# Kernel optimization log

Hardware: AMD Instinct MI355X
Metric: run time of the kernel (lower is better)

Reference implementation:

```python
import jax, jax.numpy as jnp
import numpy as np

N = 100000      # nodes
E = 1600000     # edges (avg degree 16)
F_IN = 128      # input feature dim (lazy in_channels=-1)
HID = 256       # hidden_channels
OUT = 128       # out_channels
NCLS = 2        # final softmax classes


def _l2norm(x):
    # F.normalize(p=2, dim=-1) with eps clamp, as SAGEConv(normalize=True)
    n = jnp.linalg.norm(x, axis=-1, keepdims=True)
    return x / jnp.maximum(n, 1e-12)


def _sage(x, src, tgt, Wl, bl, Wr, n_nodes):
    # PyG SAGEConv: mean-aggregate source features at targets, then
    # out = lin_l(mean_aggr) + lin_r(x); lin_l has bias, lin_r does not.
    s = jax.ops.segment_sum(x[src], tgt, num_segments=n_nodes)          # [N, F]
    cnt = jax.ops.segment_sum(jnp.ones((src.shape[0],), x.dtype), tgt,
                              num_segments=n_nodes)                     # [N]
    mean = s / jnp.maximum(cnt, 1.0)[:, None]
    out = mean @ Wl.T + bl + x @ Wr.T
    return _l2norm(out)


def setup_inputs() -> dict:
    key = jax.random.key(0)
    ks = jax.random.split(key, 12)

    def glorot(k, o, i):
        lim = float(np.sqrt(6.0 / (o + i)))
        return jax.random.uniform(k, (o, i), jnp.float32, -lim, lim)

    return {
        "x": jax.random.normal(ks[0], (N, F_IN), jnp.float32),
        "edge_index": jax.random.randint(ks[1], (2, E), 0, N, dtype=jnp.int64),
        # conv1: SAGEConv(F_IN -> HID)
        "W1l": glorot(ks[2], HID, F_IN), "b1l": jnp.zeros((HID,), jnp.float32),
        "W1r": glorot(ks[3], HID, F_IN),
        # linear: HID -> OUT
        "Wlin": glorot(ks[4], OUT, HID), "blin": jnp.zeros((OUT,), jnp.float32),
        # conv2: SAGEConv(OUT -> OUT)
        "W2l": glorot(ks[5], OUT, OUT), "b2l": jnp.zeros((OUT,), jnp.float32),
        "W2r": glorot(ks[6], OUT, OUT),
        # linear2: OUT -> 2
        "Wlin2": glorot(ks[7], NCLS, OUT), "blin2": jnp.zeros((NCLS,), jnp.float32),
    }


def reference(x, edge_index, W1l, b1l, W1r, Wlin, blin, W2l, b2l, W2r, Wlin2, blin2):
    src, tgt = edge_index[0], edge_index[1]
    h = _sage(x, src, tgt, W1l, b1l, W1r, N)            # conv1, normalize
    h = jnp.maximum(h @ Wlin.T + blin, 0.0)             # linear + relu
    y = _sage(h, src, tgt, W2l, b2l, W2r, N)            # conv2, normalize
    logits = y @ Wlin2.T + blin2                        # linear2
    probs = jax.nn.softmax(logits, axis=1)
    return probs, y
```

## Files before the change

kernel.cpp:

```cpp
#include <hip/hip_runtime.h>
#include <hip/hip_bf16.h>
#include <hip/hip_fp8.h>

#define NN   100000
#define NE   1600000
#define NBK  196
#define BSH  9
#define EPB  8192
#define CAP  9216

typedef __attribute__((ext_vector_type(8))) short short8;
typedef __attribute__((ext_vector_type(4))) float f32x4;

__device__ __forceinline__ ushort f2bf(float f) {
    union { float f; uint u; } v; v.f = f;
    uint u = v.u;
    return (ushort)((u + 0x7FFFu + ((u >> 16) & 1u)) >> 16);
}
__device__ __forceinline__ float bf2f(uint b) {
    union { uint u; float f; } v; v.u = b << 16;
    return v.f;
}
__device__ __forceinline__ float fp8f(uint byte) {
    __hip_fp8_e4m3 t; t.__x = (__hip_fp8_storage_t)(byte & 0xffu);
    return (float)t;
}
__device__ __forceinline__ uint f2fp8(float f) {
    __hip_fp8_e4m3 t(f);
    return (uint)t.__x;
}
__device__ __forceinline__ int swz(int off) { return off ^ (((off >> 9) & 7) << 4); }

__global__ __launch_bounds__(256) void bucket_hist(const int* __restrict__ tgt,
                                                   int* __restrict__ bcnt) {
    __shared__ int lh[NBK];
    int tid = threadIdx.x;
    for (int i = tid; i < NBK; i += 256) lh[i] = 0;
    __syncthreads();
    int base4 = blockIdx.x * (EPB / 4);
#pragma unroll
    for (int k = 0; k < 8; ++k) {
        int i4 = base4 + k * 256 + tid;
        if (i4 < NE / 4) {
            int4 t = ((const int4*)tgt)[i4];
            atomicAdd(&lh[t.x >> BSH], 1);
            atomicAdd(&lh[t.y >> BSH], 1);
            atomicAdd(&lh[t.z >> BSH], 1);
            atomicAdd(&lh[t.w >> BSH], 1);
        }
    }
    __syncthreads();
    for (int i = tid; i < NBK; i += 256)
        if (lh[i]) atomicAdd(&bcnt[i], lh[i]);
}

__global__ __launch_bounds__(256) void bucket_scan(const int* __restrict__ bcnt,
                                                   int* __restrict__ bbase,
                                                   int* __restrict__ bcursor,
                                                   int* __restrict__ rowstart) {
    int t = threadIdx.x;
    int v = (t < NBK) ? bcnt[t] : 0;
    int lane = t & 63, wid = t >> 6;
    int inc = v;
#pragma unroll
    for (int off = 1; off < 64; off <<= 1) {
        int u = __shfl_up(inc, off);
        if (lane >= off) inc += u;
    }
    __shared__ int ws[4];
    if (lane == 63) ws[wid] = inc;
    __syncthreads();
    int woff = 0;
    for (int w = 0; w < wid; ++w) woff += ws[w];
    int ex = woff + inc - v;
    if (t < NBK) { bbase[t] = ex; bcursor[t] = ex; }
    if (t == NBK) bbase[NBK] = ex;
    if (t == 255) rowstart[NN] = NE;
}

__global__ __launch_bounds__(256) void bucket_scatter(const int* __restrict__ src,
                                                      const int* __restrict__ tgt,
                                                      int* __restrict__ bcursor,
                                                      uint* __restrict__ brec) {
    __shared__ int lh[NBK + 1];
    __shared__ int lcur[NBK];
    __shared__ int lbase[NBK];
    __shared__ uint lrec[EPB];
    __shared__ int ws[4];
    int tid = threadIdx.x;
    for (int i = tid; i < NBK; i += 256) lh[i] = 0;
    __syncthreads();
    int base4 = blockIdx.x * (EPB / 4);
#pragma unroll
    for (int k = 0; k < 8; ++k) {
        int i4 = base4 + k * 256 + tid;
        if (i4 < NE / 4) {
            int4 t = ((const int4*)tgt)[i4];
            atomicAdd(&lh[t.x >> BSH], 1);
            atomicAdd(&lh[t.y >> BSH], 1);
            atomicAdd(&lh[t.z >> BSH], 1);
            atomicAdd(&lh[t.w >> BSH], 1);
        }
    }
    __syncthreads();
    int v = (tid < NBK) ? lh[tid] : 0;
    int lane = tid & 63, wid = tid >> 6;
    int inc = v;
#pragma unroll
    for (int off = 1; off < 64; off <<= 1) {
        int u = __shfl_up(inc, off);
        if (lane >= off) inc += u;
    }
    if (lane == 63) ws[wid] = inc;
    __syncthreads();
    int woff = 0;
    for (int w = 0; w < wid; ++w) woff += ws[w];
    int ex = woff + inc - v;
    int nval = min(EPB, NE - blockIdx.x * EPB);
    if (tid < NBK) {
        lh[tid] = ex;
        lcur[tid] = ex;
        lbase[tid] = v ? atomicAdd(&bcursor[tid], v) : 0;
    }
    if (tid == 0) lh[NBK] = nval;
    __syncthreads();
#pragma unroll
    for (int k = 0; k < 8; ++k) {
        int i4 = base4 + k * 256 + tid;
        if (i4 < NE / 4) {
            int4 t = ((const int4*)tgt)[i4];
            int4 s = ((const int4*)src)[i4];
            int p;
            p = atomicAdd(&lcur[t.x >> BSH], 1); lrec[p] = ((uint)s.x << BSH) | (uint)(t.x & 511);
            p = atomicAdd(&lcur[t.y >> BSH], 1); lrec[p] = ((uint)s.y << BSH) | (uint)(t.y & 511);
            p = atomicAdd(&lcur[t.z >> BSH], 1); lrec[p] = ((uint)s.z << BSH) | (uint)(t.z & 511);
            p = atomicAdd(&lcur[t.w >> BSH], 1); lrec[p] = ((uint)s.w << BSH) | (uint)(t.w & 511);
        }
    }
    __syncthreads();
    for (int i = tid; i < nval; i += 256) {
        int lo = 0, hi = NBK;
        while (hi - lo > 1) { int mid = (lo + hi) >> 1; if (lh[mid] <= i) lo = mid; else hi = mid; }
        brec[lbase[lo] + (i - lh[lo])] = lrec[i];
    }
}

__global__ __launch_bounds__(256) void bucket_to_csr(const uint* __restrict__ brec,
                                                     const int* __restrict__ bbase,
                                                     int* __restrict__ rowstart,
                                                     int* __restrict__ sortedSrc) {
    __shared__ int cnt[512];
    __shared__ int cur[512];
    __shared__ int srt[CAP];
    __shared__ int ws[4];
    int b = blockIdx.x;
    int beg = bbase[b], end = bbase[b + 1];
    int len = end - beg;
    int n0 = b << BSH;
    int ncnt = min(512, NN - n0);
    int tid = threadIdx.x;
    cnt[tid] = 0; cnt[tid + 256] = 0;
    __syncthreads();
    for (int i = beg + tid; i < end; i += 256)
        atomicAdd(&cnt[brec[i] & 511u], 1);
    __syncthreads();
    int c0 = cnt[2 * tid], c1 = cnt[2 * tid + 1];
    int s = c0 + c1;
    int lane = tid & 63, wid = tid >> 6;
    int inc = s;
#pragma unroll
    for (int off = 1; off < 64; off <<= 1) {
        int u = __shfl_up(inc, off);
        if (lane >= off) inc += u;
    }
    if (lane == 63) ws[wid] = inc;
    __syncthreads();
    int woff = 0;
    for (int w = 0; w < wid; ++w) woff += ws[w];
    int ex = woff + inc - s;
    cur[2 * tid] = ex; cur[2 * tid + 1] = ex + c0;
    if (2 * tid < ncnt)     rowstart[n0 + 2 * tid]     = beg + ex;
    if (2 * tid + 1 < ncnt) rowstart[n0 + 2 * tid + 1] = beg + ex + c0;
    __syncthreads();
    if (len <= CAP) {
        for (int i = beg + tid; i < end; i += 256) {
            uint r = brec[i];
            int p = atomicAdd(&cur[r & 511u], 1);
            srt[p] = (int)(r >> BSH);
        }
        __syncthreads();
        for (int i = tid; i < len; i += 256)
            sortedSrc[beg + i] = srt[i];
    } else {
        for (int i = beg + tid; i < end; i += 256) {
            uint r = brec[i];
            int p = atomicAdd(&cur[r & 511u], 1);
            sortedSrc[beg + p] = (int)(r >> BSH);
        }
    }
}

__global__ __launch_bounds__(256) void gather_mean8(const uchar* __restrict__ t8,
                                                    const int* __restrict__ rowstart,
                                                    const int* __restrict__ sortedSrc,
                                                    ushort* __restrict__ mean) {
    int node = blockIdx.x * 4 + (threadIdx.x >> 6);
    if (node >= NN) return;
    int lane = threadIdx.x & 63;
    int q = lane >> 4, l = lane & 15;
    int beg = rowstart[node], end = rowstart[node + 1];
    float a0 = 0.f, a1 = 0.f, a2 = 0.f, a3 = 0.f;
    float a4 = 0.f, a5 = 0.f, a6 = 0.f, a7 = 0.f;
    float b0 = 0.f, b1 = 0.f, b2 = 0.f, b3 = 0.f;
    float b4 = 0.f, b5 = 0.f, b6 = 0.f, b7 = 0.f;
#define ACCA(v) { a0 += fp8f(v.x);       a1 += fp8f(v.x >> 8); \
                  a2 += fp8f(v.x >> 16); a3 += fp8f(v.x >> 24); \
                  a4 += fp8f(v.y);       a5 += fp8f(v.y >> 8); \
                  a6 += fp8f(v.y >> 16); a7 += fp8f(v.y >> 24); }
#define ACCB(v) { b0 += fp8f(v.x);       b1 += fp8f(v.x >> 8); \
                  b2 += fp8f(v.x >> 16); b3 += fp8f(v.x >> 24); \
                  b4 += fp8f(v.y);       b5 += fp8f(v.y >> 8); \
                  b6 += fp8f(v.y >> 16); b7 += fp8f(v.y >> 24); }
    int i = beg + q;
    for (; i + 4 < end; i += 8) {
        int s0 = sortedSrc[i];
        int s1 = sortedSrc[i + 4];
        uint2 v0 = *(const uint2*)&t8[(size_t)s0 * 128 + l * 8];
        uint2 v1 = *(const uint2*)&t8[(size_t)s1 * 128 + l * 8];
        ACCA(v0) ACCB(v1)
    }
    if (i < end) {
        int s0 = sortedSrc[i];
        uint2 v0 = *(const uint2*)&t8[(size_t)s0 * 128 + l * 8];
        ACCA(v0)
    }
#undef ACCA
#undef ACCB
    a0 += b0; a1 += b1; a2 += b2; a3 += b3;
    a4 += b4; a5 += b5; a6 += b6; a7 += b7;
#define CMB(a) a += __shfl_xor(a, 32); a += __shfl_xor(a, 16);
    CMB(a0) CMB(a1) CMB(a2) CMB(a3) CMB(a4) CMB(a5) CMB(a6) CMB(a7)
#undef CMB
    if (lane < 16) {
        float id = 1.0f / fmaxf((float)(end - beg), 1.0f);
        ushort p[8];
        p[0] = f2bf(a0 * id); p[1] = f2bf(a1 * id);
        p[2] = f2bf(a2 * id); p[3] = f2bf(a3 * id);
        p[4] = f2bf(a4 * id); p[5] = f2bf(a5 * id);
        p[6] = f2bf(a6 * id); p[7] = f2bf(a7 * id);
        *(uint4*)&mean[(size_t)node * 128 + l * 8] = *(uint4*)p;
    }
}

__global__ __launch_bounds__(256) void prep_w(const float* __restrict__ W1l,
                                              const float* __restrict__ W1r,
                                              const float* __restrict__ Wlin,
                                              const float* __restrict__ W2l,
                                              const float* __restrict__ W2r,
                                              ushort* __restrict__ Wcat1,
                                              ushort* __restrict__ Wlinb,
                                              ushort* __restrict__ Wcat2) {
    int i = blockIdx.x * 256 + threadIdx.x;
    if (i < 65536) {
        int e = i & 7, d = (i >> 3) & 63, g = (i >> 9) & 31, ch = i >> 14;
        int col = d & 15, kg = d >> 4, ks = g & 7, nt = g >> 3;
        int row = ch * 64 + nt * 16 + col;
        int k = ks * 32 + kg * 8 + e;
        float v = (k < 128) ? W1l[row * 128 + k] : W1r[row * 128 + k - 128];
        Wcat1[i] = f2bf(v);
    } else if (i < 98304) {
        int j = i - 65536;
        int e = j & 7, d = (j >> 3) & 63, g = (j >> 9) & 31, ch = j >> 14;
        int col = d & 15, kg = d >> 4, ks = g & 7, nt = g >> 3;
        int row = ch * 64 + nt * 16 + col;
        int k = ks * 32 + kg * 8 + e;
        Wlinb[j] = f2bf(Wlin[row * 256 + k]);
    } else {
        int j = i - 98304;
        int e = j & 7, d = (j >> 3) & 63, g = (j >> 9) & 31, ch = j >> 14;
        int col = d & 15, kg = d >> 4, ks = g & 7, nt = g >> 3;
        int row = ch * 64 + nt * 16 + col;
        int k = ks * 32 + kg * 8 + e;
        float v = (k < 128) ? W2l[row * 128 + k] : W2r[row * 128 + k - 128];
        Wcat2[j] = f2bf(v);
    }
}

__global__ __launch_bounds__(256) void xcvt(const float* __restrict__ x,
                                            ushort* __restrict__ xbf,
                                            uchar* __restrict__ x8) {
    int i = blockIdx.x * 256 + threadIdx.x;
    float4 v = ((const float4*)x)[i];
    ushort4 p;
    p.x = f2bf(v.x); p.y = f2bf(v.y); p.z = f2bf(v.z); p.w = f2bf(v.w);
    ((ushort4*)xbf)[i] = p;
    uint q = f2fp8(v.x) | (f2fp8(v.y) << 8) | (f2fp8(v.z) << 16) | (f2fp8(v.w) << 24);
    ((uint*)x8)[i] = q;
}

__global__ __launch_bounds__(256) void conv1lin_mfma(const ushort* __restrict__ mean,
                                                     const ushort* __restrict__ xbf,
                                                     const ushort* __restrict__ Wcat,
                                                     const float* __restrict__ bias1,
                                                     const ushort* __restrict__ Wlin,
                                                     const float* __restrict__ blin,
                                                     ushort* __restrict__ hr,
                                                     uchar* __restrict__ hr8) {
    __shared__ char As[64 * 512];
    __shared__ char Bs[64 * 512];
    int m0 = blockIdx.x * 64;
    int tid = threadIdx.x;
    for (int c = tid; c < 2048; c += 256) {
        int m = c >> 5, kc = c & 31;
        int mm = min(m0 + m, NN - 1);
        uint4 v = (kc < 16) ? *(const uint4*)&mean[(size_t)mm * 128 + kc * 8]
                            : *(const uint4*)&xbf[(size_t)mm * 128 + (kc - 16) * 8];
        *(uint4*)(As + swz(m * 512 + kc * 16)) = v;
    }
    __syncthreads();

    int lane = tid & 63, wave = tid >> 6;
    int col = lane & 15, kg = lane >> 4;
    int mym = wave * 16 + col;
    short8 a[8];
#pragma unroll
    for (int ks = 0; ks < 8; ++ks)
        a[ks] = *(const short8*)(As + swz(mym * 512 + (ks * 32 + kg * 8) * 2));

    f32x4 acc[16];
    for (int ch = 0; ch < 4; ++ch) {
        if (ch) __syncthreads();
        for (int j = tid; j < 2048; j += 256)
            ((uint4*)Bs)[j] = ((const uint4*)(Wcat + (size_t)ch * 16384))[j];
        __syncthreads();
#pragma unroll
        for (int nt = 0; nt < 4; ++nt) {
            f32x4 c = {0.f, 0.f, 0.f, 0.f};
#pragma unroll
            for (int ks = 0; ks < 8; ++ks)
                c = __builtin_amdgcn_mfma_f32_16x16x32_bf16(
                    a[ks], *(const short8*)(Bs + ((nt * 8 + ks) * 64 + lane) * 16), c, 0, 0, 0);
            acc[ch * 4 + nt] = c;
        }
    }
    float ssq[4] = {0.f, 0.f, 0.f, 0.f};
#pragma unroll
    for (int i = 0; i < 16; ++i) {
        float b = bias1[i * 16 + col];
#pragma unroll
        for (int r = 0; r < 4; ++r) {
            acc[i][r] += b;
            ssq[r] += acc[i][r] * acc[i][r];
        }
    }
#pragma unroll
    for (int off = 1; off < 16; off <<= 1)
#pragma unroll
        for (int r = 0; r < 4; ++r) ssq[r] += __shfl_xor(ssq[r], off);
    float rn[4];
#pragma unroll
    for (int r = 0; r < 4; ++r) rn[r] = 1.0f / fmaxf(sqrtf(ssq[r]), 1e-12f);
#pragma unroll
    for (int i = 0; i < 16; ++i) {
        int chan = i * 16 + col;
#pragma unroll
        for (int r = 0; r < 4; ++r)
            *(ushort*)(As + swz((wave * 16 + kg * 4 + r) * 512 + chan * 2)) = f2bf(acc[i][r] * rn[r]);
    }
    short8 a2[8];
#pragma unroll
    for (int ks = 0; ks < 8; ++ks)
        a2[ks] = *(const short8*)(As + swz(mym * 512 + (ks * 32 + kg * 8) * 2));
    f32x4 acc2[8];
    for (int lc = 0; lc < 2; ++lc) {
        __syncthreads();
        for (int j = tid; j < 2048; j += 256)
            ((uint4*)Bs)[j] = ((const uint4*)(Wlin + (size_t)lc * 16384))[j];
        __syncthreads();
#pragma unroll
        for (int nt = 0; nt < 4; ++nt) {
            f32x4 c = {0.f, 0.f, 0.f, 0.f};
#pragma unroll
            for (int ks = 0; ks < 8; ++ks)
                c = __builtin_amdgcn_mfma_f32_16x16x32_bf16(
                    a2[ks], *(const short8*)(Bs + ((nt * 8 + ks) * 64 + lane) * 16), c, 0, 0, 0);
            acc2[lc * 4 + nt] = c;
        }
    }
#pragma unroll
    for (int i = 0; i < 8; ++i) {
        int chan = i * 16 + col;
        float b = blin[chan];
#pragma unroll
        for (int r = 0; r < 4; ++r) {
            int node = m0 + wave * 16 + kg * 4 + r;
            if (node < NN) {
                float v = fmaxf(acc2[i][r] + b, 0.f);
                hr[(size_t)node * 128 + chan] = f2bf(v);
                hr8[(size_t)node * 128 + chan] = (uchar)f2fp8(v);
            }
        }
    }
}

__global__ __launch_bounds__(256) void conv2_mfma(const ushort* __restrict__ mean,
                                                  const ushort* __restrict__ hr,
                                                  const ushort* __restrict__ Wcat,
                                                  const float* __restrict__ bias,
                                                  const float* __restrict__ Wlin2,
                                                  const float* __restrict__ blin2,
                                                  float* __restrict__ probs,
                                                  float* __restrict__ yout) {
    __shared__ char As[64 * 512];
    __shared__ char Bs[64 * 512];
    int m0 = blockIdx.x * 64;
    int tid = threadIdx.x;
    for (int c = tid; c < 2048; c += 256) {
        int m = c >> 5, kc = c & 31;
        int mm = min(m0 + m, NN - 1);
        uint4 v = (kc < 16) ? *(const uint4*)&mean[(size_t)mm * 128 + kc * 8]
                            : *(const uint4*)&hr[(size_t)mm * 128 + (kc - 16) * 8];
        *(uint4*)(As + swz(m * 512 + kc * 16)) = v;
    }
    __syncthreads();

    int lane = tid & 63, wave = tid >> 6;
    int col = lane & 15, kg = lane >> 4;
    int mym = wave * 16 + col;
    short8 a[8];
#pragma unroll
    for (int ks = 0; ks < 8; ++ks)
        a[ks] = *(const short8*)(As + swz(mym * 512 + (ks * 32 + kg * 8) * 2));

    f32x4 acc[8];
    for (int ch = 0; ch < 2; ++ch) {
        if (ch) __syncthreads();
        for (int j = tid; j < 2048; j += 256)
            ((uint4*)Bs)[j] = ((const uint4*)(Wcat + (size_t)ch * 16384))[j];
        __syncthreads();
#pragma unroll
        for (int nt = 0; nt < 4; ++nt) {
            f32x4 c = {0.f, 0.f, 0.f, 0.f};
#pragma unroll
            for (int ks = 0; ks < 8; ++ks)
                c = __builtin_amdgcn_mfma_f32_16x16x32_bf16(
                    a[ks], *(const short8*)(Bs + ((nt * 8 + ks) * 64 + lane) * 16), c, 0, 0, 0);
            acc[ch * 4 + nt] = c;
        }
    }
    float ssq[4] = {0.f, 0.f, 0.f, 0.f};
#pragma unroll
    for (int i = 0; i < 8; ++i) {
        float b = bias[i * 16 + col];
#pragma unroll
        for (int r = 0; r < 4; ++r) {
            acc[i][r] += b;
            ssq[r] += acc[i][r] * acc[i][r];
        }
    }
#pragma unroll
    for (int off = 1; off < 16; off <<= 1)
#pragma unroll
        for (int r = 0; r < 4; ++r) ssq[r] += __shfl_xor(ssq[r], off);
    float rn[4], p0[4] = {0.f,0.f,0.f,0.f}, p1[4] = {0.f,0.f,0.f,0.f};
#pragma unroll
    for (int r = 0; r < 4; ++r) rn[r] = 1.0f / fmaxf(sqrtf(ssq[r]), 1e-12f);
#pragma unroll
    for (int i = 0; i < 8; ++i) {
        int chan = i * 16 + col;
        float w0 = Wlin2[chan], w1 = Wlin2[128 + chan];
#pragma unroll
        for (int r = 0; r < 4; ++r) {
            float yv = acc[i][r] * rn[r];
            acc[i][r] = yv;
            p0[r] += yv * w0;
            p1[r] += yv * w1;
        }
    }
#pragma unroll
    for (int off = 1; off < 16; off <<= 1)
#pragma unroll
        for (int r = 0; r < 4; ++r) { p0[r] += __shfl_xor(p0[r], off); p1[r] += __shfl_xor(p1[r], off); }
#pragma unroll
    for (int r = 0; r < 4; ++r) {
        int node = m0 + wave * 16 + kg * 4 + r;
        if (node < NN) {
#pragma unroll
            for (int i = 0; i < 8; ++i)
                yout[(size_t)node * 128 + i * 16 + col] = acc[i][r];
            if (col == 0) {
                float l0 = p0[r] + blin2[0], l1 = p1[r] + blin2[1];
                float mx = fmaxf(l0, l1);
                float e0 = expf(l0 - mx), e1 = expf(l1 - mx);
                float inv = 1.0f / (e0 + e1);
                probs[(size_t)node * 2 + 0] = e0 * inv;
                probs[(size_t)node * 2 + 1] = e1 * inv;
            }
        }
    }
}

extern "C" void kernel_launch(void* const* d_in, const int* in_sizes, int n_in,
                              void* d_out, int out_size, void* d_ws, size_t ws_size,
                              hipStream_t stream) {
    const float* x     = (const float*)d_in[0];
    const int*   ei    = (const int*)d_in[1];
    const int*   src   = ei;
    const int*   tgt   = ei + NE;
    const float* W1l   = (const float*)d_in[2];
    const float* b1l   = (const float*)d_in[3];
    const float* W1r   = (const float*)d_in[4];
    const float* Wlin  = (const float*)d_in[5];
    const float* blin  = (const float*)d_in[6];
    const float* W2l   = (const float*)d_in[7];
    const float* b2l   = (const float*)d_in[8];
    const float* W2r   = (const float*)d_in[9];
    const float* Wlin2 = (const float*)d_in[10];
    const float* blin2 = (const float*)d_in[11];

    float* probs = (float*)d_out;
    float* y     = (float*)d_out + 2 * NN;

    int*    bcnt      = (int*)d_ws;
    int*    bbase     = bcnt + NBK;
    int*    bcursor   = bbase + NBK + 1;
    int*    rowstart  = bcursor + NBK;
    uint*   brec      = (uint*)(rowstart + NN + 1);
    int*    sortedSrc = (int*)(brec + NE);
    ushort* Wcat1     = (ushort*)(sortedSrc + NE);
    ushort* Wlinb     = Wcat1 + 65536;
    ushort* Wcat2     = Wlinb + 32768;
    ushort* xbf       = Wcat2 + 32768;
    ushort* hr        = xbf + (size_t)NN * 128;
    ushort* mean      = hr + (size_t)NN * 128;
    uchar*  x8        = (uchar*)(mean + (size_t)NN * 128);
    uchar*  hr8       = x8 + (size_t)NN * 128;

    const int NEB = (NE + EPB - 1) / EPB;

    hipMemsetAsync(bcnt, 0, sizeof(int) * NBK, stream);

    prep_w<<<512, 256, 0, stream>>>(W1l, W1r, Wlin, W2l, W2r, Wcat1, Wlinb, Wcat2);
    xcvt<<<NN * 32 / 256, 256, 0, stream>>>(x, xbf, x8);

    bucket_hist<<<NEB, 256, 0, stream>>>(tgt, bcnt);
    bucket_scan<<<1, 256, 0, stream>>>(bcnt, bbase, bcursor, rowstart);
    bucket_scatter<<<NEB, 256, 0, stream>>>(src, tgt, bcursor, brec);
    bucket_to_csr<<<NBK, 256, 0, stream>>>(brec, bbase, rowstart, sortedSrc);

    gather_mean8<<<(NN + 3) / 4, 256, 0, stream>>>(x8, rowstart, sortedSrc, mean);
    conv1lin_mfma<<<(NN + 63) / 64, 256, 0, stream>>>(mean, xbf, Wcat1, b1l,
                                                      Wlinb, blin, hr, hr8);
    gather_mean8<<<(NN + 3) / 4, 256, 0, stream>>>(hr8, rowstart, sortedSrc, mean);
    conv2_mfma<<<(NN + 63) / 64, 256, 0, stream>>>(mean, hr, Wcat2, b2l,
                                                   Wlin2, blin2, probs, y);
}
```

Baseline: 309.6 us.

## Stage weight tiles via direct global-to-LDS loads and split fp8 output conversion

Result: faster. 294.2 us (-5.0%).

```diff
diff --git a/kernel.cpp b/kernel.cpp
--- a/kernel.cpp
+++ b/kernel.cpp
@@ -11,6 +11,8 @@
 
 typedef __attribute__((ext_vector_type(8))) short short8;
 typedef __attribute__((ext_vector_type(4))) float f32x4;
+typedef __attribute__((address_space(3))) uint  lds_uint;
+typedef __attribute__((address_space(1))) const uint glb_uint;
 
 __device__ __forceinline__ ushort f2bf(float f) {
     union { float f; uint u; } v; v.f = f;
@@ -30,6 +32,17 @@
     return (uint)t.__x;
 }
 __device__ __forceinline__ int swz(int off) { return off ^ (((off >> 9) & 7) << 4); }
+
+__device__ __forceinline__ void stageB(const ushort* __restrict__ W, char* Bs,
+                                       int wave, int lane) {
+#pragma unroll
+    for (int k = 0; k < 8; ++k) {
+        int base = k * 256 + wave * 64;
+        __builtin_amdgcn_global_load_lds(
+            (glb_uint*)(W + (size_t)(base + lane) * 8),
+            (lds_uint*)(Bs + base * 16), 16, 0, 0);
+    }
+}
 
 __global__ __launch_bounds__(256) void bucket_hist(const int* __restrict__ tgt,
                                                    int* __restrict__ bcnt) {
@@ -298,18 +311,31 @@
     ((uint*)x8)[i] = q;
 }
 
+__global__ __launch_bounds__(256) void cvt8(const ushort* __restrict__ hr,
+                                            uchar* __restrict__ hr8) {
+    int i = blockIdx.x * 256 + threadIdx.x;
+    uint4 v = ((const uint4*)hr)[i];
+    uint lo = f2fp8(bf2f(v.x & 0xffffu)) | (f2fp8(bf2f(v.x >> 16)) << 8) |
+              (f2fp8(bf2f(v.y & 0xffffu)) << 16) | (f2fp8(bf2f(v.y >> 16)) << 24);
+    uint hi = f2fp8(bf2f(v.z & 0xffffu)) | (f2fp8(bf2f(v.z >> 16)) << 8) |
+              (f2fp8(bf2f(v.w & 0xffffu)) << 16) | (f2fp8(bf2f(v.w >> 16)) << 24);
+    uint2 o; o.x = lo; o.y = hi;
+    ((uint2*)hr8)[i] = o;
+}
+
 __global__ __launch_bounds__(256) void conv1lin_mfma(const ushort* __restrict__ mean,
                                                      const ushort* __restrict__ xbf,
                                                      const ushort* __restrict__ Wcat,
                                                      const float* __restrict__ bias1,
                                                      const ushort* __restrict__ Wlin,
                                                      const float* __restrict__ blin,
-                                                     ushort* __restrict__ hr,
-                                                     uchar* __restrict__ hr8) {
+                                                     ushort* __restrict__ hr) {
     __shared__ char As[64 * 512];
     __shared__ char Bs[64 * 512];
     int m0 = blockIdx.x * 64;
     int tid = threadIdx.x;
+    int lane = tid & 63, wave = tid >> 6;
+    stageB(Wcat, Bs, wave, lane);
     for (int c = tid; c < 2048; c += 256) {
         int m = c >> 5, kc = c & 31;
         int mm = min(m0 + m, NN - 1);
@@ -319,7 +345,6 @@
     }
     __syncthreads();
 
-    int lane = tid & 63, wave = tid >> 6;
     int col = lane & 15, kg = lane >> 4;
     int mym = wave * 16 + col;
     short8 a[8];
@@ -329,10 +354,11 @@
 
     f32x4 acc[16];
     for (int ch = 0; ch < 4; ++ch) {
-        if (ch) __syncthreads();
-        for (int j = tid; j < 2048; j += 256)
-            ((uint4*)Bs)[j] = ((const uint4*)(Wcat + (size_t)ch * 16384))[j];
-        __syncthreads();
+        if (ch) {
+            __syncthreads();
+            stageB(Wcat + (size_t)ch * 16384, Bs, wave, lane);
+            __syncthreads();
+        }
 #pragma unroll
         for (int nt = 0; nt < 4; ++nt) {
             f32x4 c = {0.f, 0.f, 0.f, 0.f};
@@ -374,8 +400,7 @@
     f32x4 acc2[8];
     for (int lc = 0; lc < 2; ++lc) {
         __syncthreads();
-        for (int j = tid; j < 2048; j += 256)
-            ((uint4*)Bs)[j] = ((const uint4*)(Wlin + (size_t)lc * 16384))[j];
+        stageB(Wlin + (size_t)lc * 16384, Bs, wave, lane);
         __syncthreads();
 #pragma unroll
         for (int nt = 0; nt < 4; ++nt) {
@@ -394,11 +419,8 @@
 #pragma unroll
         for (int r = 0; r < 4; ++r) {
             int node = m0 + wave * 16 + kg * 4 + r;
-            if (node < NN) {
-                float v = fmaxf(acc2[i][r] + b, 0.f);
-                hr[(size_t)node * 128 + chan] = f2bf(v);
-                hr8[(size_t)node * 128 + chan] = (uchar)f2fp8(v);
-            }
+            if (node < NN)
+                hr[(size_t)node * 128 + chan] = f2bf(fmaxf(acc2[i][r] + b, 0.f));
         }
     }
 }
@@ -415,6 +437,8 @@
     __shared__ char Bs[64 * 512];
     int m0 = blockIdx.x * 64;
     int tid = threadIdx.x;
+    int lane = tid & 63, wave = tid >> 6;
+    stageB(Wcat, Bs, wave, lane);
     for (int c = tid; c < 2048; c += 256) {
         int m = c >> 5, kc = c & 31;
         int mm = min(m0 + m, NN - 1);
@@ -424,7 +448,6 @@
     }
     __syncthreads();
 
-    int lane = tid & 63, wave = tid >> 6;
     int col = lane & 15, kg = lane >> 4;
     int mym = wave * 16 + col;
     short8 a[8];
@@ -434,10 +457,11 @@
 
     f32x4 acc[8];
     for (int ch = 0; ch < 2; ++ch) {
-        if (ch) __syncthreads();
-        for (int j = tid; j < 2048; j += 256)
-            ((uint4*)Bs)[j] = ((const uint4*)(Wcat + (size_t)ch * 16384))[j];
-        __syncthreads();
+        if (ch) {
+            __syncthreads();
+            stageB(Wcat + (size_t)ch * 16384, Bs, wave, lane);
+            __syncthreads();
+        }
 #pragma unroll
         for (int nt = 0; nt < 4; ++nt) {
             f32x4 c = {0.f, 0.f, 0.f, 0.f};
@@ -550,7 +574,8 @@
 
     gather_mean8<<<(NN + 3) / 4, 256, 0, stream>>>(x8, rowstart, sortedSrc, mean);
     conv1lin_mfma<<<(NN + 63) / 64, 256, 0, stream>>>(mean, xbf, Wcat1, b1l,
-                                                      Wlinb, blin, hr, hr8);
+                                                      Wlinb, blin, hr);
+    cvt8<<<NN * 128 / 8 / 256, 256, 0, stream>>>(hr, hr8);
     gather_mean8<<<(NN + 3) / 4, 256, 0, stream>>>(hr8, rowstart, sortedSrc, mean);
     conv2_mfma<<<(NN + 63) / 64, 256, 0, stream>>>(mean, hr, Wcat2, b2l,
                                                    Wlin2, blin2, probs, y);
```
